# Kernel optimization log

Hardware: AMD Instinct MI355X
Metric: run time of the kernel (lower is better)

## Reference

```python
import jax, jax.numpy as jnp
import numpy as np

N = 50000
E = 800000
D_IN = 128
D_H = 128
D_OUT = 128
EPS = 1e-5


def setup_inputs() -> dict:
    key = jax.random.key(0)
    ks = jax.random.split(key, 16)
    s = 1.0 / np.sqrt(D_IN)
    inp = {
        "x": jax.random.normal(ks[0], (N, D_IN), dtype=jnp.float32),
        "src": jax.random.randint(ks[1], (E,), 0, N, dtype=jnp.int32),
        "dst": jax.random.randint(ks[2], (E,), 0, N, dtype=jnp.int32),
        # SAGEConv layer 1 (in->hidden): fc_self, fc_neigh, bias
        "Ws1": jax.random.uniform(ks[3], (D_IN, D_H), jnp.float32, -s, s),
        "Wn1": jax.random.uniform(ks[4], (D_IN, D_H), jnp.float32, -s, s),
        "b1": jnp.zeros((D_H,), jnp.float32),
        # BN1
        "gamma1": jnp.ones((D_H,), jnp.float32),
        "beta1": jnp.zeros((D_H,), jnp.float32),
        # SAGEConv layer 2 (hidden->hidden)
        "Ws2": jax.random.uniform(ks[5], (D_H, D_H), jnp.float32, -s, s),
        "Wn2": jax.random.uniform(ks[6], (D_H, D_H), jnp.float32, -s, s),
        "b2": jnp.zeros((D_H,), jnp.float32),
        # BN2
        "gamma2": jnp.ones((D_H,), jnp.float32),
        "beta2": jnp.zeros((D_H,), jnp.float32),
        # SAGEConv layer 3 (hidden->out)
        "Ws3": jax.random.uniform(ks[7], (D_H, D_OUT), jnp.float32, -s, s),
        "Wn3": jax.random.uniform(ks[8], (D_H, D_OUT), jnp.float32, -s, s),
        "b3": jnp.zeros((D_OUT,), jnp.float32),
    }
    return inp


def _sage_conv(x, src, dst, Ws, Wn, b):
    # mean aggregation of neighbor (src) features onto dst nodes
    agg = jax.ops.segment_sum(x[src], dst, num_segments=N)  # [N, d]
    deg = jax.ops.segment_sum(jnp.ones((E,), x.dtype), dst, num_segments=N)
    h_neigh = agg / jnp.maximum(deg, 1.0)[:, None]  # isolated nodes -> 0
    return x @ Ws + h_neigh @ Wn + b


def _batch_norm(h, gamma, beta):
    mu = jnp.mean(h, axis=0)
    var = jnp.mean(jnp.square(h - mu), axis=0)  # biased var (torch BN)
    return (h - mu) * jax.lax.rsqrt(var + EPS) * gamma + beta


def reference(x, src, dst, Ws1, Wn1, b1, gamma1, beta1,
              Ws2, Wn2, b2, gamma2, beta2, Ws3, Wn3, b3):
    h = jax.nn.relu(_batch_norm(_sage_conv(x, src, dst, Ws1, Wn1, b1), gamma1, beta1))
    # dropout is identity at inference
    h = jax.nn.relu(_batch_norm(_sage_conv(h, src, dst, Ws2, Wn2, b2), gamma2, beta2))
    return _sage_conv(h, src, dst, Ws3, Wn3, b3)
```

## Files before the change

kernel.cpp:

```cpp
#include <hip/hip_runtime.h>

#define N_NODES 50000
#define NEDGE   800000
#define D       128
#define EPS     1e-5f

typedef __attribute__((ext_vector_type(8))) short bf16x8;
typedef __attribute__((ext_vector_type(4))) float f32x4;
typedef __attribute__((ext_vector_type(8))) unsigned short u16x8;

__device__ inline uint32_t bfhi(float f) {
    uint32_t u = __float_as_uint(f);
    u += 0x7fffu + ((u >> 16) & 1u);
    return u >> 16;
}
__device__ inline float bff(uint32_t h) { return __uint_as_float(h << 16); }

__global__ __launch_bounds__(256) void k_deg(const int* __restrict__ dst,
                                             int* __restrict__ degi) {
    int e = blockIdx.x * 256 + threadIdx.x;
    if (e < NEDGE) atomicAdd(&degi[dst[e]], 1);
}

__global__ __launch_bounds__(256) void k_scan1(const int* __restrict__ degi,
                                               int* __restrict__ offs,
                                               int* __restrict__ bsum) {
    __shared__ int s[256];
    int tid = threadIdx.x;
    int i = blockIdx.x * 256 + tid;
    int v = (i < N_NODES) ? degi[i] : 0;
    s[tid] = v;
    __syncthreads();
    for (int d = 1; d < 256; d <<= 1) {
        int t = (tid >= d) ? s[tid - d] : 0;
        __syncthreads();
        s[tid] += t;
        __syncthreads();
    }
    if (i < N_NODES) offs[i] = s[tid] - v;
    if (tid == 255) bsum[blockIdx.x] = s[255];
}

__global__ __launch_bounds__(256) void k_scan2(int* __restrict__ bsum, int nb) {
    __shared__ int s[256];
    int tid = threadIdx.x;
    int v = (tid < nb) ? bsum[tid] : 0;
    s[tid] = v;
    __syncthreads();
    for (int d = 1; d < 256; d <<= 1) {
        int t = (tid >= d) ? s[tid - d] : 0;
        __syncthreads();
        s[tid] += t;
        __syncthreads();
    }
    if (tid < nb) bsum[tid] = s[tid] - v;
}

__global__ __launch_bounds__(256) void k_scan3(const int* __restrict__ degi,
                                               const int* __restrict__ bsum,
                                               int* __restrict__ offs,
                                               int* __restrict__ cursor,
                                               float* __restrict__ invdeg) {
    int i = blockIdx.x * 256 + threadIdx.x;
    if (i < N_NODES) {
        int o = offs[i] + bsum[blockIdx.x];
        offs[i] = o;
        cursor[i] = o;
        int dg = degi[i];
        invdeg[i] = 1.0f / (float)(dg > 0 ? dg : 1);
    }
    if (i == 0 && blockIdx.x == 0) offs[N_NODES] = NEDGE;
}

__global__ __launch_bounds__(256) void k_fill(const int* __restrict__ src,
                                              const int* __restrict__ dst,
                                              int* __restrict__ cursor,
                                              int* __restrict__ csr) {
    int e = blockIdx.x * 256 + threadIdx.x;
    if (e < NEDGE) {
        int p = atomicAdd(&cursor[dst[e]], 1);
        csr[p] = src[e];
    }
}

__global__ __launch_bounds__(256) void k_tobf16(const float* __restrict__ X,
                                                unsigned short* __restrict__ XB) {
    int t = blockIdx.x * 256 + threadIdx.x;
    if (t >= (N_NODES * D) / 8) return;
    const float* p = X + (size_t)t * 8;
    float4 a = *reinterpret_cast<const float4*>(p);
    float4 b = *reinterpret_cast<const float4*>(p + 4);
    u16x8 o;
    o[0] = (unsigned short)bfhi(a.x); o[1] = (unsigned short)bfhi(a.y);
    o[2] = (unsigned short)bfhi(a.z); o[3] = (unsigned short)bfhi(a.w);
    o[4] = (unsigned short)bfhi(b.x); o[5] = (unsigned short)bfhi(b.y);
    o[6] = (unsigned short)bfhi(b.z); o[7] = (unsigned short)bfhi(b.w);
    *reinterpret_cast<u16x8*>(XB + (size_t)t * 8) = o;
}

__global__ __launch_bounds__(256) void k_agg(const unsigned short* __restrict__ XB,
                                             const int* __restrict__ offs,
                                             const int* __restrict__ csr,
                                             const float* __restrict__ invdeg,
                                             const float* __restrict__ bnscale,
                                             const float* __restrict__ bnshift,
                                             int useBn,
                                             float* __restrict__ HN) {
    int n = blockIdx.x * 16 + (threadIdx.x >> 4);
    if (n >= N_NODES) return;
    int c = (threadIdx.x & 15) * 8;

    float sc[8], sh[8];
    if (useBn) {
        float4 s0 = *reinterpret_cast<const float4*>(bnscale + c);
        float4 s1 = *reinterpret_cast<const float4*>(bnscale + c + 4);
        float4 h0 = *reinterpret_cast<const float4*>(bnshift + c);
        float4 h1 = *reinterpret_cast<const float4*>(bnshift + c + 4);
        sc[0] = s0.x; sc[1] = s0.y; sc[2] = s0.z; sc[3] = s0.w;
        sc[4] = s1.x; sc[5] = s1.y; sc[6] = s1.z; sc[7] = s1.w;
        sh[0] = h0.x; sh[1] = h0.y; sh[2] = h0.z; sh[3] = h0.w;
        sh[4] = h1.x; sh[5] = h1.y; sh[6] = h1.z; sh[7] = h1.w;
    }

    int e0 = offs[n], e1 = offs[n + 1];
    float acc[8];
#pragma unroll
    for (int i = 0; i < 8; ++i) acc[i] = 0.f;

    for (int e = e0; e < e1; ++e) {
        int s = csr[e];
        u16x8 v = *reinterpret_cast<const u16x8*>(XB + (size_t)s * D + c);
        if (useBn) {
#pragma unroll
            for (int i = 0; i < 8; ++i)
                acc[i] += fmaxf(bff((unsigned short)v[i]) * sc[i] + sh[i], 0.f);
        } else {
#pragma unroll
            for (int i = 0; i < 8; ++i)
                acc[i] += bff((unsigned short)v[i]);
        }
    }
    float id = invdeg[n];
    float4 o0 = {acc[0] * id, acc[1] * id, acc[2] * id, acc[3] * id};
    float4 o1 = {acc[4] * id, acc[5] * id, acc[6] * id, acc[7] * id};
    *reinterpret_cast<float4*>(HN + (size_t)n * D + c) = o0;
    *reinterpret_cast<float4*>(HN + (size_t)n * D + c + 4) = o1;
}

__global__ __launch_bounds__(256) void k_wprep(const float* __restrict__ W0,
                                               const float* __restrict__ W1,
                                               const float* __restrict__ W2,
                                               const float* __restrict__ W3,
                                               const float* __restrict__ W4,
                                               const float* __restrict__ W5,
                                               unsigned short* __restrict__ wt) {
    int mat = blockIdx.x >> 6;
    const float* srcs[6] = {W0, W1, W2, W3, W4, W5};
    const float* W = srcs[mat];
    int t = (blockIdx.x & 63) * 256 + threadIdx.x;
    int k = t >> 7;
    int n = t & 127;
    float w = W[k * 128 + n];
    uint32_t h = bfhi(w);
    uint32_t l = bfhi(w - bff(h));
    unsigned short* base = wt + (size_t)mat * 32768;
    base[n * 128 + k] = (unsigned short)h;
    base[16384 + n * 128 + k] = (unsigned short)l;
}

#define LDS_RS 272
#define LDS_PLANE (64 * LDS_RS)
__global__ __launch_bounds__(512) void k_mm(const float* __restrict__ Xf,
                                            const unsigned short* __restrict__ Xhi,
                                            const unsigned short* __restrict__ Xlo,
                                            const float* __restrict__ HN,
                                            const unsigned short* __restrict__ WsT,
                                            const unsigned short* __restrict__ WnT,
                                            const float* __restrict__ bias,
                                            const float* __restrict__ bnscale,
                                            const float* __restrict__ bnshift,
                                            int mode,
                                            float* __restrict__ OUTf,
                                            unsigned short* __restrict__ OUThi,
                                            unsigned short* __restrict__ OUTlo,
                                            int outFp32,
                                            int doStats,
                                            float* __restrict__ sums) {
    __shared__ __align__(16) unsigned char smem[4 * LDS_PLANE];

    const int tid = threadIdx.x;
    const int lane = tid & 63;
    const int wave = tid >> 6;
    const int row0 = blockIdx.x * 64;
    const int mlo = lane & 15;
    const int g = lane >> 4;
    const int col = (wave << 4) + mlo;
    const int kb = g * 8;

    bf16x8 wsh[4], wsl[4], wnh[4], wnl[4];
#pragma unroll
    for (int kc = 0; kc < 4; ++kc) {
        int ko = kc * 32 + kb;
        wsh[kc] = *reinterpret_cast<const bf16x8*>(WsT + (size_t)col * 128 + ko);
        wsl[kc] = *reinterpret_cast<const bf16x8*>(WsT + 16384 + (size_t)col * 128 + ko);
        wnh[kc] = *reinterpret_cast<const bf16x8*>(WnT + (size_t)col * 128 + ko);
        wnl[kc] = *reinterpret_cast<const bf16x8*>(WnT + 16384 + (size_t)col * 128 + ko);
    }

#pragma unroll
    for (int uu = 0; uu < 2; ++uu) {
        int u = tid + uu * 512;
        int r = u >> 4;
        int ks = u & 15;
        int grow = row0 + r;
        float f[8], a[8];
        if (grow < N_NODES) {
            if (mode == 0) {
                const float* xp = Xf + (size_t)grow * D + ks * 8;
                float4 x0 = *reinterpret_cast<const float4*>(xp);
                float4 x1 = *reinterpret_cast<const float4*>(xp + 4);
                f[0] = x0.x; f[1] = x0.y; f[2] = x0.z; f[3] = x0.w;
                f[4] = x1.x; f[5] = x1.y; f[6] = x1.z; f[7] = x1.w;
            } else {
                u16x8 hi = *reinterpret_cast<const u16x8*>(Xhi + (size_t)grow * D + ks * 8);
                u16x8 lo = *reinterpret_cast<const u16x8*>(Xlo + (size_t)grow * D + ks * 8);
                float4 s0 = *reinterpret_cast<const float4*>(bnscale + ks * 8);
                float4 s1 = *reinterpret_cast<const float4*>(bnscale + ks * 8 + 4);
                float4 h0 = *reinterpret_cast<const float4*>(bnshift + ks * 8);
                float4 h1 = *reinterpret_cast<const float4*>(bnshift + ks * 8 + 4);
                float scv[8] = {s0.x, s0.y, s0.z, s0.w, s1.x, s1.y, s1.z, s1.w};
                float shv[8] = {h0.x, h0.y, h0.z, h0.w, h1.x, h1.y, h1.z, h1.w};
#pragma unroll
                for (int i = 0; i < 8; ++i) {
                    float v = bff((unsigned short)hi[i]) + bff((unsigned short)lo[i]);
                    f[i] = fmaxf(v * scv[i] + shv[i], 0.f);
                }
            }
            const float* ap = HN + (size_t)grow * D + ks * 8;
            float4 a0 = *reinterpret_cast<const float4*>(ap);
            float4 a1 = *reinterpret_cast<const float4*>(ap + 4);
            a[0] = a0.x; a[1] = a0.y; a[2] = a0.z; a[3] = a0.w;
            a[4] = a1.x; a[5] = a1.y; a[6] = a1.z; a[7] = a1.w;
        } else {
#pragma unroll
            for (int i = 0; i < 8; ++i) { f[i] = 0.f; a[i] = 0.f; }
        }
        int base = r * LDS_RS + ks * 16;
        uint32_t h8[8];
        int4 vhi, vlo;
#pragma unroll
        for (int i = 0; i < 8; ++i) h8[i] = bfhi(f[i]);
        vhi.x = h8[0] | (h8[1] << 16); vhi.y = h8[2] | (h8[3] << 16);
        vhi.z = h8[4] | (h8[5] << 16); vhi.w = h8[6] | (h8[7] << 16);
        {
            uint32_t l0 = bfhi(f[0] - bff(h8[0])), l1 = bfhi(f[1] - bff(h8[1]));
            uint32_t l2 = bfhi(f[2] - bff(h8[2])), l3 = bfhi(f[3] - bff(h8[3]));
            uint32_t l4 = bfhi(f[4] - bff(h8[4])), l5 = bfhi(f[5] - bff(h8[5]));
            uint32_t l6 = bfhi(f[6] - bff(h8[6])), l7 = bfhi(f[7] - bff(h8[7]));
            vlo.x = l0 | (l1 << 16); vlo.y = l2 | (l3 << 16);
            vlo.z = l4 | (l5 << 16); vlo.w = l6 | (l7 << 16);
        }
        *reinterpret_cast<int4*>(smem + 0 * LDS_PLANE + base) = vhi;
        *reinterpret_cast<int4*>(smem + 1 * LDS_PLANE + base) = vlo;
#pragma unroll
        for (int i = 0; i < 8; ++i) h8[i] = bfhi(a[i]);
        vhi.x = h8[0] | (h8[1] << 16); vhi.y = h8[2] | (h8[3] << 16);
        vhi.z = h8[4] | (h8[5] << 16); vhi.w = h8[6] | (h8[7] << 16);
        {
            uint32_t l0 = bfhi(a[0] - bff(h8[0])), l1 = bfhi(a[1] - bff(h8[1]));
            uint32_t l2 = bfhi(a[2] - bff(h8[2])), l3 = bfhi(a[3] - bff(h8[3]));
            uint32_t l4 = bfhi(a[4] - bff(h8[4])), l5 = bfhi(a[5] - bff(h8[5]));
            uint32_t l6 = bfhi(a[6] - bff(h8[6])), l7 = bfhi(a[7] - bff(h8[7]));
            vlo.x = l0 | (l1 << 16); vlo.y = l2 | (l3 << 16);
            vlo.z = l4 | (l5 << 16); vlo.w = l6 | (l7 << 16);
        }
        *reinterpret_cast<int4*>(smem + 2 * LDS_PLANE + base) = vhi;
        *reinterpret_cast<int4*>(smem + 3 * LDS_PLANE + base) = vlo;
    }
    __syncthreads();

    f32x4 acc[4];
#pragma unroll
    for (int s = 0; s < 4; ++s) acc[s] = (f32x4){0.f, 0.f, 0.f, 0.f};

#pragma unroll
    for (int kc = 0; kc < 4; ++kc) {
        int ksr = kc * 4 + g;
        int ko = ksr * 16;
#pragma unroll
        for (int s = 0; s < 4; ++s) {
            int ad = (s * 16 + mlo) * LDS_RS + ko;
            bf16x8 xh = *reinterpret_cast<const bf16x8*>(smem + 0 * LDS_PLANE + ad);
            bf16x8 xl = *reinterpret_cast<const bf16x8*>(smem + 1 * LDS_PLANE + ad);
            bf16x8 ah = *reinterpret_cast<const bf16x8*>(smem + 2 * LDS_PLANE + ad);
            bf16x8 al = *reinterpret_cast<const bf16x8*>(smem + 3 * LDS_PLANE + ad);
            acc[s] = __builtin_amdgcn_mfma_f32_16x16x32_bf16(xh, wsh[kc], acc[s], 0, 0, 0);
            acc[s] = __builtin_amdgcn_mfma_f32_16x16x32_bf16(xh, wsl[kc], acc[s], 0, 0, 0);
            acc[s] = __builtin_amdgcn_mfma_f32_16x16x32_bf16(xl, wsh[kc], acc[s], 0, 0, 0);
            acc[s] = __builtin_amdgcn_mfma_f32_16x16x32_bf16(ah, wnh[kc], acc[s], 0, 0, 0);
            acc[s] = __builtin_amdgcn_mfma_f32_16x16x32_bf16(ah, wnl[kc], acc[s], 0, 0, 0);
            acc[s] = __builtin_amdgcn_mfma_f32_16x16x32_bf16(al, wnh[kc], acc[s], 0, 0, 0);
        }
    }

    float bcol = bias[col];
    float cs = 0.f, cq = 0.f;
#pragma unroll
    for (int s = 0; s < 4; ++s) {
#pragma unroll
        for (int r = 0; r < 4; ++r) {
            int grow = row0 + s * 16 + g * 4 + r;
            if (grow < N_NODES) {
                float v = acc[s][r] + bcol;
                if (outFp32) {
                    OUTf[(size_t)grow * D + col] = v;
                } else {
                    uint32_t h = bfhi(v);
                    OUThi[(size_t)grow * D + col] = (unsigned short)h;
                    OUTlo[(size_t)grow * D + col] = (unsigned short)bfhi(v - bff(h));
                }
                cs += v; cq += v * v;
            }
        }
    }
    if (doStats) {
        cs += __shfl_xor(cs, 16); cs += __shfl_xor(cs, 32);
        cq += __shfl_xor(cq, 16); cq += __shfl_xor(cq, 32);
        if (lane < 16) {
            atomicAdd(&sums[col], cs);
            atomicAdd(&sums[128 + col], cq);
        }
    }
}

__global__ void k_bnfin(const float* __restrict__ sums,
                        const float* __restrict__ gamma,
                        const float* __restrict__ beta,
                        float* __restrict__ scale,
                        float* __restrict__ shift) {
    int c = threadIdx.x;
    const float invN = 1.0f / (float)N_NODES;
    float mu = sums[c] * invN;
    float var = sums[128 + c] * invN - mu * mu;
    float s = gamma[c] * rsqrtf(var + EPS);
    scale[c] = s;
    shift[c] = beta[c] - mu * s;
}

extern "C" void kernel_launch(void* const* d_in, const int* in_sizes, int n_in,
                              void* d_out, int out_size, void* d_ws, size_t ws_size,
                              hipStream_t stream) {
    const float* x   = (const float*)d_in[0];
    const int*   src = (const int*)d_in[1];
    const int*   dst = (const int*)d_in[2];
    const float* Ws1 = (const float*)d_in[3];
    const float* Wn1 = (const float*)d_in[4];
    const float* b1  = (const float*)d_in[5];
    const float* g1  = (const float*)d_in[6];
    const float* be1 = (const float*)d_in[7];
    const float* Ws2 = (const float*)d_in[8];
    const float* Wn2 = (const float*)d_in[9];
    const float* b2  = (const float*)d_in[10];
    const float* g2  = (const float*)d_in[11];
    const float* be2 = (const float*)d_in[12];
    const float* Ws3 = (const float*)d_in[13];
    const float* Wn3 = (const float*)d_in[14];
    const float* b3  = (const float*)d_in[15];
    float* out = (float*)d_out;

    char* p = (char*)d_ws;
    auto alloc = [&](size_t bytes) -> char* {
        char* r = p;
        p += (bytes + 255) & ~(size_t)255;
        return r;
    };
    float* hn   = (float*)alloc((size_t)N_NODES * D * 4);
    unsigned short* xb   = (unsigned short*)alloc((size_t)N_NODES * D * 2);
    unsigned short* h1hi = (unsigned short*)alloc((size_t)N_NODES * D * 2);
    unsigned short* h1lo = (unsigned short*)alloc((size_t)N_NODES * D * 2);
    unsigned short* h2hi = (unsigned short*)alloc((size_t)N_NODES * D * 2);
    unsigned short* h2lo = (unsigned short*)alloc((size_t)N_NODES * D * 2);
    int*   csr    = (int*)alloc((size_t)NEDGE * 4);
    int*   offs   = (int*)alloc((size_t)(N_NODES + 1) * 4);
    int*   cursor = (int*)alloc((size_t)N_NODES * 4);
    int*   degi   = (int*)alloc((size_t)N_NODES * 4);
    float* invdeg = (float*)alloc((size_t)N_NODES * 4);
    int*   bsum   = (int*)alloc(1024);
    float* sums   = (float*)alloc(256 * 4);
    float* scale  = (float*)alloc(128 * 4);
    float* shift  = (float*)alloc(128 * 4);
    unsigned short* wt = (unsigned short*)alloc((size_t)6 * 32768 * 2);

    const int NB_E = (NEDGE + 255) / 256;
    const int NB_N = (N_NODES + 255) / 256;
    const int NB_A = (N_NODES + 15) / 16;
    const int NB_M = (N_NODES + 63) / 64;
    const int NB_T = (N_NODES * D / 8 + 255) / 256;

    const unsigned short* WsT1 = wt + 0 * 32768;
    const unsigned short* WnT1 = wt + 1 * 32768;
    const unsigned short* WsT2 = wt + 2 * 32768;
    const unsigned short* WnT2 = wt + 3 * 32768;
    const unsigned short* WsT3 = wt + 4 * 32768;
    const unsigned short* WnT3 = wt + 5 * 32768;

    k_wprep<<<384, 256, 0, stream>>>(Ws1, Wn1, Ws2, Wn2, Ws3, Wn3, wt);
    hipMemsetAsync(degi, 0, (size_t)N_NODES * 4, stream);
    k_deg<<<NB_E, 256, 0, stream>>>(dst, degi);
    k_scan1<<<NB_N, 256, 0, stream>>>(degi, offs, bsum);
    k_scan2<<<1, 256, 0, stream>>>(bsum, NB_N);
    k_scan3<<<NB_N, 256, 0, stream>>>(degi, bsum, offs, cursor, invdeg);
    k_fill<<<NB_E, 256, 0, stream>>>(src, dst, cursor, csr);
    k_tobf16<<<NB_T, 256, 0, stream>>>(x, xb);

    k_agg<<<NB_A, 256, 0, stream>>>(xb, offs, csr, invdeg, scale, shift, 0, hn);
    hipMemsetAsync(sums, 0, 256 * 4, stream);
    k_mm<<<NB_M, 512, 0, stream>>>(x, h1hi, h1lo, hn, WsT1, WnT1, b1, scale, shift,
                                   0, out, h1hi, h1lo, 0, 1, sums);
    k_bnfin<<<1, 128, 0, stream>>>(sums, g1, be1, scale, shift);

    k_agg<<<NB_A, 256, 0, stream>>>(h1hi, offs, csr, invdeg, scale, shift, 1, hn);
    hipMemsetAsync(sums, 0, 256 * 4, stream);
    k_mm<<<NB_M, 512, 0, stream>>>(x, h1hi, h1lo, hn, WsT2, WnT2, b2, scale, shift,
                                   1, out, h2hi, h2lo, 0, 1, sums);
    k_bnfin<<<1, 128, 0, stream>>>(sums, g2, be2, scale, shift);

    k_agg<<<NB_A, 256, 0, stream>>>(h2hi, offs, csr, invdeg, scale, shift, 1, hn);
    k_mm<<<NB_M, 512, 0, stream>>>(x, h2hi, h2lo, hn, WsT3, WnT3, b3, scale, shift,
                                   1, out, h1hi, h1lo, 1, 0, sums);
}
```

Before: 441.0 us.

## Split bf16 features into column halves and drop LDS staging in GEMM

Stores the bf16 feature tables in two planes of 64 columns each. The aggregation kernel gathers one half per block, with blocks interleaved so each half's gather set is smaller and more cache-friendly, and it unrolls the edge loop by two with dual accumulators. The GEMM kernel now splits output columns across two blocks of 256 threads and builds MFMA operands directly in registers from global loads, removing LDS staging and the barrier. The cost is that each input row is loaded and converted twice, once per column-half block.

```diff
diff --git a/kernel.cpp b/kernel.cpp
--- a/kernel.cpp
+++ b/kernel.cpp
@@ -4,6 +4,7 @@
 #define NEDGE   800000
 #define D       128
 #define EPS     1e-5f
+#define NHALF   ((size_t)N_NODES * 64)
 
 typedef __attribute__((ext_vector_type(8))) short bf16x8;
 typedef __attribute__((ext_vector_type(4))) float f32x4;
@@ -87,7 +88,9 @@
                                                 unsigned short* __restrict__ XB) {
     int t = blockIdx.x * 256 + threadIdx.x;
     if (t >= (N_NODES * D) / 8) return;
-    const float* p = X + (size_t)t * 8;
+    int n = t >> 4;
+    int c8 = (t & 15) * 8;
+    const float* p = X + (size_t)n * D + c8;
     float4 a = *reinterpret_cast<const float4*>(p);
     float4 b = *reinterpret_cast<const float4*>(p + 4);
     u16x8 o;
@@ -95,7 +98,8 @@
     o[2] = (unsigned short)bfhi(a.z); o[3] = (unsigned short)bfhi(a.w);
     o[4] = (unsigned short)bfhi(b.x); o[5] = (unsigned short)bfhi(b.y);
     o[6] = (unsigned short)bfhi(b.z); o[7] = (unsigned short)bfhi(b.w);
-    *reinterpret_cast<u16x8*>(XB + (size_t)t * 8) = o;
+    int half = c8 >> 6;
+    *reinterpret_cast<u16x8*>(XB + (size_t)half * NHALF + (size_t)n * 64 + (c8 & 63)) = o;
 }
 
 __global__ __launch_bounds__(256) void k_agg(const unsigned short* __restrict__ XB,
@@ -106,16 +110,22 @@
                                              const float* __restrict__ bnshift,
                                              int useBn,
                                              float* __restrict__ HN) {
-    int n = blockIdx.x * 16 + (threadIdx.x >> 4);
+    int bid = blockIdx.x;
+    int half = (bid >> 2) & 1;
+    int nb = (bid >> 3) * 4 + (bid & 3);
+    if (nb >= 1563) return;
+    int n = nb * 32 + (threadIdx.x >> 3);
     if (n >= N_NODES) return;
-    int c = (threadIdx.x & 15) * 8;
+    int c = (threadIdx.x & 7) * 8;
+    int gc = half * 64 + c;
+    const unsigned short* XH = XB + (size_t)half * NHALF;
 
     float sc[8], sh[8];
     if (useBn) {
-        float4 s0 = *reinterpret_cast<const float4*>(bnscale + c);
-        float4 s1 = *reinterpret_cast<const float4*>(bnscale + c + 4);
-        float4 h0 = *reinterpret_cast<const float4*>(bnshift + c);
-        float4 h1 = *reinterpret_cast<const float4*>(bnshift + c + 4);
+        float4 s0 = *reinterpret_cast<const float4*>(bnscale + gc);
+        float4 s1 = *reinterpret_cast<const float4*>(bnscale + gc + 4);
+        float4 h0 = *reinterpret_cast<const float4*>(bnshift + gc);
+        float4 h1 = *reinterpret_cast<const float4*>(bnshift + gc + 4);
         sc[0] = s0.x; sc[1] = s0.y; sc[2] = s0.z; sc[3] = s0.w;
         sc[4] = s1.x; sc[5] = s1.y; sc[6] = s1.z; sc[7] = s1.w;
         sh[0] = h0.x; sh[1] = h0.y; sh[2] = h0.z; sh[3] = h0.w;
@@ -123,28 +133,49 @@
     }
 
     int e0 = offs[n], e1 = offs[n + 1];
-    float acc[8];
-#pragma unroll
-    for (int i = 0; i < 8; ++i) acc[i] = 0.f;
-
-    for (int e = e0; e < e1; ++e) {
-        int s = csr[e];
-        u16x8 v = *reinterpret_cast<const u16x8*>(XB + (size_t)s * D + c);
+    float a0[8], a1[8];
+#pragma unroll
+    for (int i = 0; i < 8; ++i) { a0[i] = 0.f; a1[i] = 0.f; }
+
+    int e = e0;
+    for (; e + 2 <= e1; e += 2) {
+        int s0i = csr[e], s1i = csr[e + 1];
+        u16x8 v0 = *reinterpret_cast<const u16x8*>(XH + (size_t)s0i * 64 + c);
+        u16x8 v1 = *reinterpret_cast<const u16x8*>(XH + (size_t)s1i * 64 + c);
         if (useBn) {
 #pragma unroll
+            for (int i = 0; i < 8; ++i) {
+                a0[i] += fmaxf(bff((unsigned short)v0[i]) * sc[i] + sh[i], 0.f);
+                a1[i] += fmaxf(bff((unsigned short)v1[i]) * sc[i] + sh[i], 0.f);
+            }
+        } else {
+#pragma unroll
+            for (int i = 0; i < 8; ++i) {
+                a0[i] += bff((unsigned short)v0[i]);
+                a1[i] += bff((unsigned short)v1[i]);
+            }
+        }
+    }
+    if (e < e1) {
+        int s0i = csr[e];
+        u16x8 v0 = *reinterpret_cast<const u16x8*>(XH + (size_t)s0i * 64 + c);
+        if (useBn) {
+#pragma unroll
             for (int i = 0; i < 8; ++i)
-                acc[i] += fmaxf(bff((unsigned short)v[i]) * sc[i] + sh[i], 0.f);
+                a0[i] += fmaxf(bff((unsigned short)v0[i]) * sc[i] + sh[i], 0.f);
         } else {
 #pragma unroll
             for (int i = 0; i < 8; ++i)
-                acc[i] += bff((unsigned short)v[i]);
+                a0[i] += bff((unsigned short)v0[i]);
         }
     }
     float id = invdeg[n];
-    float4 o0 = {acc[0] * id, acc[1] * id, acc[2] * id, acc[3] * id};
-    float4 o1 = {acc[4] * id, acc[5] * id, acc[6] * id, acc[7] * id};
-    *reinterpret_cast<float4*>(HN + (size_t)n * D + c) = o0;
-    *reinterpret_cast<float4*>(HN + (size_t)n * D + c + 4) = o1;
+    float4 o0 = {(a0[0] + a1[0]) * id, (a0[1] + a1[1]) * id,
+                 (a0[2] + a1[2]) * id, (a0[3] + a1[3]) * id};
+    float4 o1 = {(a0[4] + a1[4]) * id, (a0[5] + a1[5]) * id,
+                 (a0[6] + a1[6]) * id, (a0[7] + a1[7]) * id};
+    *reinterpret_cast<float4*>(HN + (size_t)n * D + gc) = o0;
+    *reinterpret_cast<float4*>(HN + (size_t)n * D + gc + 4) = o1;
 }
 
 __global__ __launch_bounds__(256) void k_wprep(const float* __restrict__ W0,
@@ -168,142 +199,105 @@
     base[16384 + n * 128 + k] = (unsigned short)l;
 }
 
-#define LDS_RS 272
-#define LDS_PLANE (64 * LDS_RS)
-__global__ __launch_bounds__(512) void k_mm(const float* __restrict__ Xf,
-                                            const unsigned short* __restrict__ Xhi,
-                                            const unsigned short* __restrict__ Xlo,
-                                            const float* __restrict__ HN,
-                                            const unsigned short* __restrict__ WsT,
-                                            const unsigned short* __restrict__ WnT,
-                                            const float* __restrict__ bias,
-                                            const float* __restrict__ bnscale,
-                                            const float* __restrict__ bnshift,
-                                            int mode,
-                                            float* __restrict__ OUTf,
-                                            unsigned short* __restrict__ OUThi,
-                                            unsigned short* __restrict__ OUTlo,
-                                            int outFp32,
-                                            int doStats,
-                                            float* __restrict__ sums) {
-    __shared__ __align__(16) unsigned char smem[4 * LDS_PLANE];
-
+__global__ __launch_bounds__(256, 3) void k_mm(const float* __restrict__ Xf,
+                                               const unsigned short* __restrict__ Xhi,
+                                               const unsigned short* __restrict__ Xlo,
+                                               const float* __restrict__ HN,
+                                               const unsigned short* __restrict__ WsT,
+                                               const unsigned short* __restrict__ WnT,
+                                               const float* __restrict__ bias,
+                                               const float* __restrict__ bnscale,
+                                               const float* __restrict__ bnshift,
+                                               int mode,
+                                               float* __restrict__ OUTf,
+                                               unsigned short* __restrict__ OUThi,
+                                               unsigned short* __restrict__ OUTlo,
+                                               int outFp32,
+                                               int doStats,
+                                               float* __restrict__ sums) {
     const int tid = threadIdx.x;
     const int lane = tid & 63;
     const int wave = tid >> 6;
-    const int row0 = blockIdx.x * 64;
     const int mlo = lane & 15;
     const int g = lane >> 4;
-    const int col = (wave << 4) + mlo;
-    const int kb = g * 8;
-
-    bf16x8 wsh[4], wsl[4], wnh[4], wnl[4];
+    const int ch = blockIdx.x & 1;
+    const int row0 = (blockIdx.x >> 1) * 64;
+    const int col = ch * 64 + wave * 16 + mlo;
+    const float bcol = bias[col];
+
+    f32x4 acc[4];
+#pragma unroll
+    for (int s = 0; s < 4; ++s) acc[s] = (f32x4){0.f, 0.f, 0.f, 0.f};
+
 #pragma unroll
     for (int kc = 0; kc < 4; ++kc) {
-        int ko = kc * 32 + kb;
-        wsh[kc] = *reinterpret_cast<const bf16x8*>(WsT + (size_t)col * 128 + ko);
-        wsl[kc] = *reinterpret_cast<const bf16x8*>(WsT + 16384 + (size_t)col * 128 + ko);
-        wnh[kc] = *reinterpret_cast<const bf16x8*>(WnT + (size_t)col * 128 + ko);
-        wnl[kc] = *reinterpret_cast<const bf16x8*>(WnT + 16384 + (size_t)col * 128 + ko);
-    }
-
-#pragma unroll
-    for (int uu = 0; uu < 2; ++uu) {
-        int u = tid + uu * 512;
-        int r = u >> 4;
-        int ks = u & 15;
-        int grow = row0 + r;
-        float f[8], a[8];
-        if (grow < N_NODES) {
-            if (mode == 0) {
-                const float* xp = Xf + (size_t)grow * D + ks * 8;
-                float4 x0 = *reinterpret_cast<const float4*>(xp);
-                float4 x1 = *reinterpret_cast<const float4*>(xp + 4);
-                f[0] = x0.x; f[1] = x0.y; f[2] = x0.z; f[3] = x0.w;
-                f[4] = x1.x; f[5] = x1.y; f[6] = x1.z; f[7] = x1.w;
+        const int k0 = kc * 32 + g * 8;
+        bf16x8 wsh = *reinterpret_cast<const bf16x8*>(WsT + (size_t)col * 128 + k0);
+        bf16x8 wsl = *reinterpret_cast<const bf16x8*>(WsT + 16384 + (size_t)col * 128 + k0);
+        bf16x8 wnh = *reinterpret_cast<const bf16x8*>(WnT + (size_t)col * 128 + k0);
+        bf16x8 wnl = *reinterpret_cast<const bf16x8*>(WnT + 16384 + (size_t)col * 128 + k0);
+
+        float sc8[8], sh8[8];
+        if (mode == 1) {
+            float4 s0 = *reinterpret_cast<const float4*>(bnscale + k0);
+            float4 s1 = *reinterpret_cast<const float4*>(bnscale + k0 + 4);
+            float4 h0 = *reinterpret_cast<const float4*>(bnshift + k0);
+            float4 h1 = *reinterpret_cast<const float4*>(bnshift + k0 + 4);
+            sc8[0] = s0.x; sc8[1] = s0.y; sc8[2] = s0.z; sc8[3] = s0.w;
+            sc8[4] = s1.x; sc8[5] = s1.y; sc8[6] = s1.z; sc8[7] = s1.w;
+            sh8[0] = h0.x; sh8[1] = h0.y; sh8[2] = h0.z; sh8[3] = h0.w;
+            sh8[4] = h1.x; sh8[5] = h1.y; sh8[6] = h1.z; sh8[7] = h1.w;
+        }
+
+#pragma unroll
+        for (int s = 0; s < 4; ++s) {
+            int row = row0 + s * 16 + mlo;
+            float fx[8], fa[8];
+            if (row < N_NODES) {
+                const float* ap = HN + (size_t)row * D + k0;
+                float4 a0 = *reinterpret_cast<const float4*>(ap);
+                float4 a1 = *reinterpret_cast<const float4*>(ap + 4);
+                fa[0] = a0.x; fa[1] = a0.y; fa[2] = a0.z; fa[3] = a0.w;
+                fa[4] = a1.x; fa[5] = a1.y; fa[6] = a1.z; fa[7] = a1.w;
+                if (mode == 0) {
+                    const float* xp = Xf + (size_t)row * D + k0;
+                    float4 x0 = *reinterpret_cast<const float4*>(xp);
+                    float4 x1 = *reinterpret_cast<const float4*>(xp + 4);
+                    fx[0] = x0.x; fx[1] = x0.y; fx[2] = x0.z; fx[3] = x0.w;
+                    fx[4] = x1.x; fx[5] = x1.y; fx[6] = x1.z; fx[7] = x1.w;
+                } else {
+                    u16x8 hi = *reinterpret_cast<const u16x8*>(
+                        Xhi + (size_t)(kc >> 1) * NHALF + (size_t)row * 64 + ((kc & 1) * 32 + g * 8));
+                    u16x8 lo = *reinterpret_cast<const u16x8*>(Xlo + (size_t)row * D + k0);
+#pragma unroll
+                    for (int i = 0; i < 8; ++i) {
+                        float v = bff((unsigned short)hi[i]) + bff((unsigned short)lo[i]);
+                        fx[i] = fmaxf(v * sc8[i] + sh8[i], 0.f);
+                    }
+                }
             } else {
-                u16x8 hi = *reinterpret_cast<const u16x8*>(Xhi + (size_t)grow * D + ks * 8);
-                u16x8 lo = *reinterpret_cast<const u16x8*>(Xlo + (size_t)grow * D + ks * 8);
-                float4 s0 = *reinterpret_cast<const float4*>(bnscale + ks * 8);
-                float4 s1 = *reinterpret_cast<const float4*>(bnscale + ks * 8 + 4);
-                float4 h0 = *reinterpret_cast<const float4*>(bnshift + ks * 8);
-                float4 h1 = *reinterpret_cast<const float4*>(bnshift + ks * 8 + 4);
-                float scv[8] = {s0.x, s0.y, s0.z, s0.w, s1.x, s1.y, s1.z, s1.w};
-                float shv[8] = {h0.x, h0.y, h0.z, h0.w, h1.x, h1.y, h1.z, h1.w};
-#pragma unroll
-                for (int i = 0; i < 8; ++i) {
-                    float v = bff((unsigned short)hi[i]) + bff((unsigned short)lo[i]);
-                    f[i] = fmaxf(v * scv[i] + shv[i], 0.f);
-                }
+#pragma unroll
+                for (int i = 0; i < 8; ++i) { fx[i] = 0.f; fa[i] = 0.f; }
             }
-            const float* ap = HN + (size_t)grow * D + ks * 8;
-            float4 a0 = *reinterpret_cast<const float4*>(ap);
-            float4 a1 = *reinterpret_cast<const float4*>(ap + 4);
-            a[0] = a0.x; a[1] = a0.y; a[2] = a0.z; a[3] = a0.w;
-            a[4] = a1.x; a[5] = a1.y; a[6] = a1.z; a[7] = a1.w;
-        } else {
-#pragma unroll
-            for (int i = 0; i < 8; ++i) { f[i] = 0.f; a[i] = 0.f; }
-        }
-        int base = r * LDS_RS + ks * 16;
-        uint32_t h8[8];
-        int4 vhi, vlo;
-#pragma unroll
-        for (int i = 0; i < 8; ++i) h8[i] = bfhi(f[i]);
-        vhi.x = h8[0] | (h8[1] << 16); vhi.y = h8[2] | (h8[3] << 16);
-        vhi.z = h8[4] | (h8[5] << 16); vhi.w = h8[6] | (h8[7] << 16);
-        {
-            uint32_t l0 = bfhi(f[0] - bff(h8[0])), l1 = bfhi(f[1] - bff(h8[1]));
-            uint32_t l2 = bfhi(f[2] - bff(h8[2])), l3 = bfhi(f[3] - bff(h8[3]));
-            uint32_t l4 = bfhi(f[4] - bff(h8[4])), l5 = bfhi(f[5] - bff(h8[5]));
-            uint32_t l6 = bfhi(f[6] - bff(h8[6])), l7 = bfhi(f[7] - bff(h8[7]));
-            vlo.x = l0 | (l1 << 16); vlo.y = l2 | (l3 << 16);
-            vlo.z = l4 | (l5 << 16); vlo.w = l6 | (l7 << 16);
-        }
-        *reinterpret_cast<int4*>(smem + 0 * LDS_PLANE + base) = vhi;
-        *reinterpret_cast<int4*>(smem + 1 * LDS_PLANE + base) = vlo;
-#pragma unroll
-        for (int i = 0; i < 8; ++i) h8[i] = bfhi(a[i]);
-        vhi.x = h8[0] | (h8[1] << 16); vhi.y = h8[2] | (h8[3] << 16);
-        vhi.z = h8[4] | (h8[5] << 16); vhi.w = h8[6] | (h8[7] << 16);
-        {
-            uint32_t l0 = bfhi(a[0] - bff(h8[0])), l1 = bfhi(a[1] - bff(h8[1]));
-            uint32_t l2 = bfhi(a[2] - bff(h8[2])), l3 = bfhi(a[3] - bff(h8[3]));
-            uint32_t l4 = bfhi(a[4] - bff(h8[4])), l5 = bfhi(a[5] - bff(h8[5]));
-            uint32_t l6 = bfhi(a[6] - bff(h8[6])), l7 = bfhi(a[7] - bff(h8[7]));
-            vlo.x = l0 | (l1 << 16); vlo.y = l2 | (l3 << 16);
-            vlo.z = l4 | (l5 << 16); vlo.w = l6 | (l7 << 16);
-        }
-        *reinterpret_cast<int4*>(smem + 2 * LDS_PLANE + base) = vhi;
-        *reinterpret_cast<int4*>(smem + 3 * LDS_PLANE + base) = vlo;
-    }
-    __syncthreads();
-
-    f32x4 acc[4];
-#pragma unroll
-    for (int s = 0; s < 4; ++s) acc[s] = (f32x4){0.f, 0.f, 0.f, 0.f};
-
-#pragma unroll
-    for (int kc = 0; kc < 4; ++kc) {
-        int ksr = kc * 4 + g;
-        int ko = ksr * 16;
-#pragma unroll
-        for (int s = 0; s < 4; ++s) {
-            int ad = (s * 16 + mlo) * LDS_RS + ko;
-            bf16x8 xh = *reinterpret_cast<const bf16x8*>(smem + 0 * LDS_PLANE + ad);
-            bf16x8 xl = *reinterpret_cast<const bf16x8*>(smem + 1 * LDS_PLANE + ad);
-            bf16x8 ah = *reinterpret_cast<const bf16x8*>(smem + 2 * LDS_PLANE + ad);
-            bf16x8 al = *reinterpret_cast<const bf16x8*>(smem + 3 * LDS_PLANE + ad);
-            acc[s] = __builtin_amdgcn_mfma_f32_16x16x32_bf16(xh, wsh[kc], acc[s], 0, 0, 0);
-            acc[s] = __builtin_amdgcn_mfma_f32_16x16x32_bf16(xh, wsl[kc], acc[s], 0, 0, 0);
-            acc[s] = __builtin_amdgcn_mfma_f32_16x16x32_bf16(xl, wsh[kc], acc[s], 0, 0, 0);
-            acc[s] = __builtin_amdgcn_mfma_f32_16x16x32_bf16(ah, wnh[kc], acc[s], 0, 0, 0);
-            acc[s] = __builtin_amdgcn_mfma_f32_16x16x32_bf16(ah, wnl[kc], acc[s], 0, 0, 0);
-            acc[s] = __builtin_amdgcn_mfma_f32_16x16x32_bf16(al, wnh[kc], acc[s], 0, 0, 0);
-        }
-    }
-
-    float bcol = bias[col];
+            bf16x8 xh, xl, ah, al;
+#pragma unroll
+            for (int i = 0; i < 8; ++i) {
+                uint32_t h = bfhi(fx[i]);
+                xh[i] = (short)h;
+                xl[i] = (short)bfhi(fx[i] - bff(h));
+                uint32_t ha = bfhi(fa[i]);
+                ah[i] = (short)ha;
+                al[i] = (short)bfhi(fa[i] - bff(ha));
+            }
+            acc[s] = __builtin_amdgcn_mfma_f32_16x16x32_bf16(xh, wsh, acc[s], 0, 0, 0);
+            acc[s] = __builtin_amdgcn_mfma_f32_16x16x32_bf16(xh, wsl, acc[s], 0, 0, 0);
+            acc[s] = __builtin_amdgcn_mfma_f32_16x16x32_bf16(xl, wsh, acc[s], 0, 0, 0);
+            acc[s] = __builtin_amdgcn_mfma_f32_16x16x32_bf16(ah, wnh, acc[s], 0, 0, 0);
+            acc[s] = __builtin_amdgcn_mfma_f32_16x16x32_bf16(ah, wnl, acc[s], 0, 0, 0);
+            acc[s] = __builtin_amdgcn_mfma_f32_16x16x32_bf16(al, wnh, acc[s], 0, 0, 0);
+        }
+    }
+
     float cs = 0.f, cq = 0.f;
 #pragma unroll
     for (int s = 0; s < 4; ++s) {
@@ -316,7 +310,7 @@
                     OUTf[(size_t)grow * D + col] = v;
                 } else {
                     uint32_t h = bfhi(v);
-                    OUThi[(size_t)grow * D + col] = (unsigned short)h;
+                    OUThi[(size_t)ch * NHALF + (size_t)grow * 64 + (col & 63)] = (unsigned short)h;
                     OUTlo[(size_t)grow * D + col] = (unsigned short)bfhi(v - bff(h));
                 }
                 cs += v; cq += v * v;
@@ -393,8 +387,8 @@
 
     const int NB_E = (NEDGE + 255) / 256;
     const int NB_N = (N_NODES + 255) / 256;
-    const int NB_A = (N_NODES + 15) / 16;
-    const int NB_M = (N_NODES + 63) / 64;
+    const int NB_A = 3128;
+    const int NB_M = 2 * ((N_NODES + 63) / 64);
     const int NB_T = (N_NODES * D / 8 + 255) / 256;
 
     const unsigned short* WsT1 = wt + 0 * 32768;
@@ -415,17 +409,17 @@
 
     k_agg<<<NB_A, 256, 0, stream>>>(xb, offs, csr, invdeg, scale, shift, 0, hn);
     hipMemsetAsync(sums, 0, 256 * 4, stream);
-    k_mm<<<NB_M, 512, 0, stream>>>(x, h1hi, h1lo, hn, WsT1, WnT1, b1, scale, shift,
+    k_mm<<<NB_M, 256, 0, stream>>>(x, h1hi, h1lo, hn, WsT1, WnT1, b1, scale, shift,
                                    0, out, h1hi, h1lo, 0, 1, sums);
     k_bnfin<<<1, 128, 0, stream>>>(sums, g1, be1, scale, shift);
 
     k_agg<<<NB_A, 256, 0, stream>>>(h1hi, offs, csr, invdeg, scale, shift, 1, hn);
     hipMemsetAsync(sums, 0, 256 * 4, stream);
-    k_mm<<<NB_M, 512, 0, stream>>>(x, h1hi, h1lo, hn, WsT2, WnT2, b2, scale, shift,
+    k_mm<<<NB_M, 256, 0, stream>>>(x, h1hi, h1lo, hn, WsT2, WnT2, b2, scale, shift,
                                    1, out, h2hi, h2lo, 0, 1, sums);
     k_bnfin<<<1, 128, 0, stream>>>(sums, g2, be2, scale, shift);
 
     k_agg<<<NB_A, 256, 0, stream>>>(h2hi, offs, csr, invdeg, scale, shift, 1, hn);
-    k_mm<<<NB_M, 512, 0, stream>>>(x, h2hi, h2lo, hn, WsT3, WnT3, b3, scale, shift,
+    k_mm<<<NB_M, 256, 0, stream>>>(x, h2hi, h2lo, hn, WsT3, WnT3, b3, scale, shift,
                                    1, out, h1hi, h1lo, 1, 0, sums);
 }
```

Result: slower. 523.7 us (+18.7%).
